# Kernel optimization log

Measured on AMD Instinct MI355X. Metric: run time of the kernel, lower is better.

Reference implementation:

```python
import jax, jax.numpy as jnp
import numpy as np

B, N, S = 32, 512, 64  # batch, num_nodes, seq_len


def setup_inputs() -> dict:
    key = jax.random.key(0)
    k1, k2, k3, k4, k5 = jax.random.split(key, 5)
    global_inputs = jax.random.normal(k1, (B, N, S), dtype=jnp.float32)
    attention_states = jax.random.normal(k2, (B, S, N), dtype=jnp.float32)
    v = jax.random.normal(k3, (S,), dtype=jnp.float32)            # global_v
    attn0 = jax.random.normal(k4, (B, N), dtype=jnp.float32) * (np.sqrt(6.0 / (B + N)))  # xavier-ish init of global_attn
    W = jax.random.uniform(k5, (N, S), dtype=jnp.float32,
                           minval=-np.sqrt(6.0 / (N + S)), maxval=np.sqrt(6.0 / (N + S)))
    b = jnp.zeros((S,), dtype=jnp.float32)
    return {"global_inputs": global_inputs, "attention_states": attention_states,
            "v": v, "attn0": attn0, "W": W, "b": b}


def reference(global_inputs, attention_states, v, attn0, W, b):
    # global_inputs: [B, N, S]; attention_states (hidden): [B, S, N]
    hidden = attention_states
    inputs_t = jnp.transpose(global_inputs, (2, 0, 1))  # [S, B, N], loop over time

    def step(attn, inp):
        # attn: [B, N] recurrent attention state; inp: [B, N]
        x = attn * inp                                   # output of this step
        y = x @ W + b                                    # [B, S]
        # hidden[b,s,n] + y[b,k] -> tanh -> weighted sum over s and k
        t = jnp.tanh(hidden[:, :, :, None] + y[:, None, None, :])  # [B, S, N, S]
        s = jnp.einsum('bsnk,k->bn', t, v)               # sum over dims 1 and 3 weighted by v
        a = jax.nn.softmax(s, axis=1)                    # softmax over nodes
        return a, x

    _, outs = jax.lax.scan(step, attn0, inputs_t)        # outs: [S, B, N]
    return outs
```

## Files before the change

kernel.cpp:

```cpp
#include <hip/hip_runtime.h>

#define BB   32
#define NN   512
#define SS   64
#define TPB  1024
#define P    16
#define YMAX 0.8f
#define PI_F 3.14159265358979f

__device__ __forceinline__ float rcp_fast(float x) { return __builtin_amdgcn_rcpf(x); }

__global__ void __launch_bounds__(512)
transpose_gin(const float* __restrict__ gin, float* __restrict__ gt) {
    __shared__ float tile[64][65];
    const int b  = blockIdx.x >> 3;
    const int n0 = (blockIdx.x & 7) << 6;
    const int c  = threadIdx.x & 63;
    const int r  = threadIdx.x >> 6;
#pragma unroll
    for (int j = 0; j < 8; ++j) {
        int nl = r * 8 + j;
        tile[nl][c] = gin[b * NN * SS + (n0 + nl) * SS + c];
    }
    __syncthreads();
#pragma unroll
    for (int j = 0; j < 8; ++j) {
        int s = r * 8 + j;
        gt[b * SS * NN + s * NN + n0 + c] = tile[c][s];
    }
}

__global__ void __launch_bounds__(TPB)
spatial_attn_kernel(const float* __restrict__ gin,
                    const float* __restrict__ gt,
                    int use_t,
                    const float* __restrict__ hid,
                    const float* __restrict__ v,
                    const float* __restrict__ attn0,
                    const float* __restrict__ W,
                    const float* __restrict__ bias,
                    float* __restrict__ out)
{
    const int b    = blockIdx.x;
    const int t    = threadIdx.x;
    const int lane = t & 63;
    const int w    = t >> 6;

    __shared__ float x_lds[NN];
    __shared__ float yred[16][SS];
    __shared__ float mom[SS][P + 1];
    __shared__ float m_lds[P];
    __shared__ float ms[8], ss_[8];
    __shared__ float ctab[P * P];
    __shared__ float gscr[P][NN];

    float wr[32];
#pragma unroll
    for (int j = 0; j < 32; ++j)
        wr[j] = W[(w * 32 + j) * SS + lane];

    if (t < P * P) {
        int p = t >> 4, i = t & 15;
        float cs = __cosf(PI_F * (i + 0.5f) * (float)p / (float)P);
        ctab[t] = cs * ((p == 0) ? (1.0f / P) : (2.0f / P));
    }
    if (t < 8) { ms[t] = 0.f; ss_[t] = 0.125f; }
    const float vreg = (t < SS) ? v[t] : 0.f;
    const float bk   = (t < SS) ? bias[t] : 0.f;

    float u[P];
#pragma unroll
    for (int i = 0; i < P; ++i) {
        float yi = YMAX * __cosf(PI_F * (i + 0.5f) / (float)P);
        float e  = __expf(2.f * yi);
        u[i] = 1.f - 2.f * rcp_fast(e + 1.f);
    }

    const int n  = t & 511;
    const int hs = t >> 9;
    float g[P];
#pragma unroll
    for (int i = 0; i < P; ++i) g[i] = 0.f;
    for (int s = hs * 32; s < hs * 32 + 32; ++s) {
        float H  = hid[b * SS * NN + s * NN + n];
        float e2 = __expf(2.f * H);
        float T  = 1.f - 2.f * rcp_fast(e2 + 1.f);
#pragma unroll
        for (int i = 0; i < P; ++i)
            g[i] += (T + u[i]) * rcp_fast(fmaf(T, u[i], 1.f));
    }
    if (hs) {
#pragma unroll
        for (int i = 0; i < P; ++i) gscr[i][n] = g[i];
    }

    float xu_reg = 0.f, inp_nxt = 0.f;
    if (t < NN) {
        float inp0 = use_t ? gt[(size_t)b * SS * NN + t]
                           : gin[(size_t)b * NN * SS + t * SS];
        xu_reg = attn0[b * NN + t] * inp0;
        x_lds[t] = xu_reg;
        inp_nxt = use_t ? gt[(size_t)b * SS * NN + NN + t]
                        : gin[(size_t)b * NN * SS + t * SS + 1];
    }
    __syncthreads();

    float c[P];
    if (t < NN) {
#pragma unroll
        for (int i = 0; i < P; ++i) g[i] += gscr[i][n];
#pragma unroll
        for (int p = 0; p < P; ++p) {
            float a = 0.f;
#pragma unroll
            for (int i = 0; i < P; ++i) a = fmaf(ctab[p * P + i], g[i], a);
            c[p] = a;
        }
    }

    for (int tau = 0; tau < SS - 1; ++tau) {
        float mM = ms[0];
#pragma unroll
        for (int i = 1; i < 8; ++i) mM = fmaxf(mM, ms[i]);
        float Tn = 0.f;
#pragma unroll
        for (int i = 0; i < 8; ++i) Tn = fmaf(__expf(ms[i] - mM), ss_[i], Tn);
        float rT = rcp_fast(Tn);

        const int nx = (tau + 2 < SS) ? tau + 2 : SS - 1;
        float inp_pf = 0.f;
        if (t < NN)
            inp_pf = use_t ? gt[(size_t)b * SS * NN + nx * NN + t]
                           : gin[(size_t)b * NN * SS + t * SS + nx];

        if (t < NN)
            out[(size_t)tau * BB * NN + b * NN + t] =
                xu_reg * (__expf(ms[t >> 6] - mM) * rT);

        {
            float scl = __expf(ms[w >> 1] - mM) * rT;
            float p = 0.f;
#pragma unroll
            for (int j = 0; j < 32; ++j)
                p = fmaf(x_lds[(w << 5) + j], wr[j], p);
            yred[w][lane] = p * scl;
        }
        __syncthreads();

        if (t < SS) {
            float y = bk;
#pragma unroll
            for (int g2 = 0; g2 < 16; ++g2) y += yred[g2][t];
            float yt = y * (1.0f / YMAX);
            yt = fminf(1.f, fmaxf(-1.f, yt));
            float t0 = 1.f, t1 = yt;
            mom[t][0] = vreg;
            mom[t][1] = vreg * yt;
#pragma unroll
            for (int p = 2; p < P; ++p) {
                float t2 = fmaf(2.f * yt, t1, -t0);
                mom[t][p] = vreg * t2;
                t0 = t1; t1 = t2;
            }
            const int pp = t >> 2, q = t & 3;
            float a = 0.f;
#pragma unroll
            for (int j = 0; j < 16; ++j) a += mom[q + 4 * j][pp];
            a += __shfl_xor(a, 1);
            a += __shfl_xor(a, 2);
            if (q == 0) m_lds[pp] = a;
        }
        __syncthreads();

        if (t < NN) {
            float s = 0.f;
#pragma unroll
            for (int p = 0; p < P; ++p) s = fmaf(c[p], m_lds[p], s);
            float m = s;
#pragma unroll
            for (int off = 1; off < 64; off <<= 1)
                m = fmaxf(m, __shfl_xor(m, off));
            float e = __expf(s - m);
            float S = e;
#pragma unroll
            for (int off = 1; off < 64; off <<= 1)
                S += __shfl_xor(S, off);
            xu_reg = e * inp_nxt;
            x_lds[t] = xu_reg;
            if (lane == 0) ms[t >> 6] = m;
            if (lane == 1) ss_[t >> 6] = S;
        }
        inp_nxt = inp_pf;
        __syncthreads();
    }

    {
        float mM = ms[0];
#pragma unroll
        for (int i = 1; i < 8; ++i) mM = fmaxf(mM, ms[i]);
        float Tn = 0.f;
#pragma unroll
        for (int i = 0; i < 8; ++i) Tn = fmaf(__expf(ms[i] - mM), ss_[i], Tn);
        float rT = rcp_fast(Tn);
        if (t < NN)
            out[(size_t)(SS - 1) * BB * NN + b * NN + t] =
                xu_reg * (__expf(ms[t >> 6] - mM) * rT);
    }
}

extern "C" void kernel_launch(void* const* d_in, const int* in_sizes, int n_in,
                              void* d_out, int out_size, void* d_ws, size_t ws_size,
                              hipStream_t stream) {
    const float* gin   = (const float*)d_in[0];
    const float* hid   = (const float*)d_in[1];
    const float* v     = (const float*)d_in[2];
    const float* attn0 = (const float*)d_in[3];
    const float* W     = (const float*)d_in[4];
    const float* bias  = (const float*)d_in[5];
    float* out = (float*)d_out;

    float* gt = (float*)d_ws;
    size_t need_t = (size_t)BB * NN * SS * 4;
    int use_t = (ws_size >= need_t) ? 1 : 0;

    if (use_t)
        transpose_gin<<<dim3(BB * 8), dim3(512), 0, stream>>>(gin, gt);
    else
        gt = (float*)gin;

    spatial_attn_kernel<<<dim3(BB), dim3(TPB), 0, stream>>>(
        gin, gt, use_t, hid, v, attn0, W, bias, out);
}
```

Measured before the change: 197.4 us.

## Replace per-step block barriers with wave-level atomic producer/consumer signalling

Each wave now owns the 32 nodes whose W rows it already holds, so it computes its own partial x·W and a per-wave softmax max and sum without waiting on the rest of the block. The three __syncthreads per time step are replaced by an LDS atomic counter: waves publish their partials, wave 0 combines them, builds the Chebyshev moments, then releases a flag that the other waves spin on with s_sleep. The aim is to shorten the serial latency chain of the 64-step recurrence. In exchange, half the lanes in each wave sit idle during the softmax step, and correctness now depends on careful memory ordering of the hand-written spin-waits.

```diff
diff --git a/kernel.cpp b/kernel.cpp
--- a/kernel.cpp
+++ b/kernel.cpp
@@ -4,6 +4,7 @@
 #define NN   512
 #define SS   64
 #define TPB  1024
+#define NW   16
 #define P    16
 #define YMAX 0.8f
 #define PI_F 3.14159265358979f
@@ -41,32 +42,36 @@
                     const float* __restrict__ bias,
                     float* __restrict__ out)
 {
-    const int b    = blockIdx.x;
-    const int t    = threadIdx.x;
-    const int lane = t & 63;
-    const int w    = t >> 6;
+    const int b     = blockIdx.x;
+    const int t     = threadIdx.x;
+    const int lane  = t & 63;
+    const int w     = t >> 6;
+    const int ln    = lane & 31;
+    const int n_own = w * 32 + ln;
 
     __shared__ float x_lds[NN];
-    __shared__ float yred[16][SS];
-    __shared__ float mom[SS][P + 1];
-    __shared__ float m_lds[P];
-    __shared__ float ms[8], ss_[8];
+    __shared__ float yred[NW][SS];
+    __shared__ float msA[NW], ssA[NW];
+    __shared__ float momt[SS][P + 1];
+    __shared__ float mco[P + NW];
     __shared__ float ctab[P * P];
     __shared__ float gscr[P][NN];
-
-    float wr[32];
-#pragma unroll
-    for (int j = 0; j < 32; ++j)
-        wr[j] = W[(w * 32 + j) * SS + lane];
-
+    __shared__ unsigned int cntA, flagA;
+
+    if (t == 0) { cntA = 0u; flagA = 0u; }
+    if (t < NW) { msA[t] = 0.f; ssA[t] = 1.0f / NW; }
     if (t < P * P) {
         int p = t >> 4, i = t & 15;
         float cs = __cosf(PI_F * (i + 0.5f) * (float)p / (float)P);
         ctab[t] = cs * ((p == 0) ? (1.0f / P) : (2.0f / P));
     }
-    if (t < 8) { ms[t] = 0.f; ss_[t] = 0.125f; }
-    const float vreg = (t < SS) ? v[t] : 0.f;
-    const float bk   = (t < SS) ? bias[t] : 0.f;
+    const float vreg = v[lane];
+    const float bk   = bias[lane];
+
+    float wr[32];
+#pragma unroll
+    for (int j = 0; j < 32; ++j)
+        wr[j] = W[(w * 32 + j) * SS + lane];
 
     float u[P];
 #pragma unroll
@@ -76,13 +81,12 @@
         u[i] = 1.f - 2.f * rcp_fast(e + 1.f);
     }
 
-    const int n  = t & 511;
-    const int hs = t >> 9;
+    const int n5 = t & 511, hs = t >> 9;
     float g[P];
 #pragma unroll
     for (int i = 0; i < P; ++i) g[i] = 0.f;
     for (int s = hs * 32; s < hs * 32 + 32; ++s) {
-        float H  = hid[b * SS * NN + s * NN + n];
+        float H  = hid[b * SS * NN + s * NN + n5];
         float e2 = __expf(2.f * H);
         float T  = 1.f - 2.f * rcp_fast(e2 + 1.f);
 #pragma unroll
@@ -91,120 +95,159 @@
     }
     if (hs) {
 #pragma unroll
-        for (int i = 0; i < P; ++i) gscr[i][n] = g[i];
-    }
-
-    float xu_reg = 0.f, inp_nxt = 0.f;
+        for (int i = 0; i < P; ++i) gscr[i][n5] = g[i];
+    }
+    __syncthreads();
     if (t < NN) {
-        float inp0 = use_t ? gt[(size_t)b * SS * NN + t]
-                           : gin[(size_t)b * NN * SS + t * SS];
-        xu_reg = attn0[b * NN + t] * inp0;
-        x_lds[t] = xu_reg;
-        inp_nxt = use_t ? gt[(size_t)b * SS * NN + NN + t]
-                        : gin[(size_t)b * NN * SS + t * SS + 1];
-    }
-    __syncthreads();
-
-    float c[P];
-    if (t < NN) {
-#pragma unroll
-        for (int i = 0; i < P; ++i) g[i] += gscr[i][n];
+#pragma unroll
+        for (int i = 0; i < P; ++i) g[i] += gscr[i][n5];
 #pragma unroll
         for (int p = 0; p < P; ++p) {
             float a = 0.f;
 #pragma unroll
             for (int i = 0; i < P; ++i) a = fmaf(ctab[p * P + i], g[i], a);
-            c[p] = a;
-        }
-    }
+            gscr[p][n5] = a;
+        }
+    }
+    __syncthreads();
+
+    float cc[P];
+    float x_t = 0.f, inp1 = 0.f, inp2 = 0.f;
+    if (lane < 32) {
+#pragma unroll
+        for (int p = 0; p < P; ++p) cc[p] = gscr[p][n_own];
+        float i0 = use_t ? gt[(size_t)b * SS * NN + n_own]
+                         : gin[(size_t)b * NN * SS + n_own * SS];
+        x_t  = attn0[b * NN + n_own] * i0;
+        inp1 = use_t ? gt[(size_t)b * SS * NN + NN + n_own]
+                     : gin[(size_t)b * NN * SS + n_own * SS + 1];
+        inp2 = use_t ? gt[(size_t)b * SS * NN + 2 * NN + n_own]
+                     : gin[(size_t)b * NN * SS + n_own * SS + 2];
+        x_lds[n_own] = x_t;
+    }
+    {
+        float yp = 0.f;
+        const float4* xv = (const float4*)&x_lds[w * 32];
+#pragma unroll
+        for (int j4 = 0; j4 < 8; ++j4) {
+            float4 q = xv[j4];
+            yp = fmaf(q.x, wr[4 * j4 + 0], yp);
+            yp = fmaf(q.y, wr[4 * j4 + 1], yp);
+            yp = fmaf(q.z, wr[4 * j4 + 2], yp);
+            yp = fmaf(q.w, wr[4 * j4 + 3], yp);
+        }
+        yred[w][lane] = yp;
+    }
+    if (lane == 0)
+        __hip_atomic_fetch_add(&cntA, 1u, __ATOMIC_RELEASE, __HIP_MEMORY_SCOPE_WORKGROUP);
 
     for (int tau = 0; tau < SS - 1; ++tau) {
-        float mM = ms[0];
-#pragma unroll
-        for (int i = 1; i < 8; ++i) mM = fmaxf(mM, ms[i]);
-        float Tn = 0.f;
-#pragma unroll
-        for (int i = 0; i < 8; ++i) Tn = fmaf(__expf(ms[i] - mM), ss_[i], Tn);
-        float rT = rcp_fast(Tn);
-
-        const int nx = (tau + 2 < SS) ? tau + 2 : SS - 1;
-        float inp_pf = 0.f;
-        if (t < NN)
-            inp_pf = use_t ? gt[(size_t)b * SS * NN + nx * NN + t]
-                           : gin[(size_t)b * NN * SS + t * SS + nx];
-
-        if (t < NN)
-            out[(size_t)tau * BB * NN + b * NN + t] =
-                xu_reg * (__expf(ms[t >> 6] - mM) * rT);
-
-        {
-            float scl = __expf(ms[w >> 1] - mM) * rT;
-            float p = 0.f;
-#pragma unroll
-            for (int j = 0; j < 32; ++j)
-                p = fmaf(x_lds[(w << 5) + j], wr[j], p);
-            yred[w][lane] = p * scl;
-        }
-        __syncthreads();
-
-        if (t < SS) {
-            float y = bk;
-#pragma unroll
-            for (int g2 = 0; g2 < 16; ++g2) y += yred[g2][t];
+        if (w == 0) {
+            const unsigned int tgt = 16u * (unsigned int)(tau + 1);
+            while (__hip_atomic_load(&cntA, __ATOMIC_ACQUIRE, __HIP_MEMORY_SCOPE_WORKGROUP) < tgt)
+                __builtin_amdgcn_s_sleep(1);
+            float mM = msA[0];
+#pragma unroll
+            for (int i = 1; i < 16; ++i) mM = fmaxf(mM, msA[i]);
+            float e16[16], T = 0.f;
+#pragma unroll
+            for (int i = 0; i < 16; ++i) {
+                e16[i] = __expf(msA[i] - mM);
+                T = fmaf(e16[i], ssA[i], T);
+            }
+            float rT = rcp_fast(T);
+            float acc = 0.f;
+#pragma unroll
+            for (int i = 0; i < 16; ++i) acc = fmaf(e16[i], yred[i][lane], acc);
+            float y  = fmaf(acc, rT, bk);
             float yt = y * (1.0f / YMAX);
             yt = fminf(1.f, fmaxf(-1.f, yt));
             float t0 = 1.f, t1 = yt;
-            mom[t][0] = vreg;
-            mom[t][1] = vreg * yt;
+            momt[lane][0] = vreg;
+            momt[lane][1] = vreg * yt;
 #pragma unroll
             for (int p = 2; p < P; ++p) {
                 float t2 = fmaf(2.f * yt, t1, -t0);
-                mom[t][p] = vreg * t2;
+                momt[lane][p] = vreg * t2;
                 t0 = t1; t1 = t2;
             }
-            const int pp = t >> 2, q = t & 3;
+            const int pp = lane >> 2, q = lane & 3;
             float a = 0.f;
 #pragma unroll
-            for (int j = 0; j < 16; ++j) a += mom[q + 4 * j][pp];
+            for (int j = 0; j < 16; ++j) a += momt[q + 4 * j][pp];
             a += __shfl_xor(a, 1);
             a += __shfl_xor(a, 2);
-            if (q == 0) m_lds[pp] = a;
-        }
-        __syncthreads();
-
-        if (t < NN) {
+            if (q == 0) mco[pp] = a;
+            if (lane < 16) mco[P + lane] = __expf(msA[lane] - mM) * rT;
+            if (lane == 0)
+                __hip_atomic_store(&flagA, (unsigned int)(tau + 1),
+                                   __ATOMIC_RELEASE, __HIP_MEMORY_SCOPE_WORKGROUP);
+        } else {
+            while (__hip_atomic_load(&flagA, __ATOMIC_ACQUIRE, __HIP_MEMORY_SCOPE_WORKGROUP)
+                   < (unsigned int)(tau + 1))
+                __builtin_amdgcn_s_sleep(1);
+        }
+
+        float inp_pf = 0.f;
+        if (lane < 32) {
+            int nx = (tau + 3 < SS) ? tau + 3 : SS - 1;
+            inp_pf = use_t ? gt[(size_t)b * SS * NN + nx * NN + n_own]
+                           : gin[(size_t)b * NN * SS + n_own * SS + nx];
+        }
+        float Mp[P];
+#pragma unroll
+        for (int p = 0; p < P; ++p) Mp[p] = mco[p];
+        const float scl_own = mco[P + w];
+        if (lane < 32) {
+            out[(size_t)tau * BB * NN + b * NN + n_own] = x_t * scl_own;
             float s = 0.f;
 #pragma unroll
-            for (int p = 0; p < P; ++p) s = fmaf(c[p], m_lds[p], s);
+            for (int p = 0; p < P; ++p) s = fmaf(cc[p], Mp[p], s);
             float m = s;
 #pragma unroll
-            for (int off = 1; off < 64; off <<= 1)
+            for (int off = 1; off < 32; off <<= 1)
                 m = fmaxf(m, __shfl_xor(m, off));
             float e = __expf(s - m);
             float S = e;
 #pragma unroll
-            for (int off = 1; off < 64; off <<= 1)
+            for (int off = 1; off < 32; off <<= 1)
                 S += __shfl_xor(S, off);
-            xu_reg = e * inp_nxt;
-            x_lds[t] = xu_reg;
-            if (lane == 0) ms[t >> 6] = m;
-            if (lane == 1) ss_[t >> 6] = S;
-        }
-        inp_nxt = inp_pf;
-        __syncthreads();
-    }
-
+            x_t = e * inp1;
+            x_lds[n_own] = x_t;
+            if (ln == 0) msA[w] = m;
+            if (ln == 1) ssA[w] = S;
+        }
+        inp1 = inp2; inp2 = inp_pf;
+        {
+            float yp = 0.f;
+            const float4* xv = (const float4*)&x_lds[w * 32];
+#pragma unroll
+            for (int j4 = 0; j4 < 8; ++j4) {
+                float4 q = xv[j4];
+                yp = fmaf(q.x, wr[4 * j4 + 0], yp);
+                yp = fmaf(q.y, wr[4 * j4 + 1], yp);
+                yp = fmaf(q.z, wr[4 * j4 + 2], yp);
+                yp = fmaf(q.w, wr[4 * j4 + 3], yp);
+            }
+            yred[w][lane] = yp;
+        }
+        if (lane == 0)
+            __hip_atomic_fetch_add(&cntA, 1u, __ATOMIC_RELEASE, __HIP_MEMORY_SCOPE_WORKGROUP);
+    }
+
+    while (__hip_atomic_load(&cntA, __ATOMIC_ACQUIRE, __HIP_MEMORY_SCOPE_WORKGROUP) < 16u * 64u)
+        __builtin_amdgcn_s_sleep(1);
     {
-        float mM = ms[0];
-#pragma unroll
-        for (int i = 1; i < 8; ++i) mM = fmaxf(mM, ms[i]);
-        float Tn = 0.f;
-#pragma unroll
-        for (int i = 0; i < 8; ++i) Tn = fmaf(__expf(ms[i] - mM), ss_[i], Tn);
-        float rT = rcp_fast(Tn);
-        if (t < NN)
-            out[(size_t)(SS - 1) * BB * NN + b * NN + t] =
-                xu_reg * (__expf(ms[t >> 6] - mM) * rT);
+        float mM = msA[0];
+#pragma unroll
+        for (int i = 1; i < 16; ++i) mM = fmaxf(mM, msA[i]);
+        float T = 0.f;
+#pragma unroll
+        for (int i = 0; i < 16; ++i) T = fmaf(__expf(msA[i] - mM), ssA[i], T);
+        float rT = rcp_fast(T);
+        if (lane < 32)
+            out[(size_t)(SS - 1) * BB * NN + b * NN + n_own] =
+                x_t * (__expf(msA[w] - mM) * rT);
     }
 }
 
```

New measurement: 211.3 us. +7.0%, slower.
